# Performance work log

Hardware: AMD Instinct MI355X
Metric: run time of the kernel (lower is better)

Reference implementation:

```python
import jax, jax.numpy as jnp
import numpy as np

D_MODEL, D_K, D_V, N_HEADS = 1024, 64, 64, 16


def setup_inputs() -> dict:
    key = jax.random.key(0)
    ks = jax.random.split(key, 8)
    B, S = 2, 2048
    s = 0.02
    return {
        "x": jax.random.normal(ks[0], (B, S, D_MODEL), dtype=jnp.float32),
        "Wq": jax.random.normal(ks[1], (D_MODEL, N_HEADS * D_K), dtype=jnp.float32) * s,
        "bq": jnp.zeros((N_HEADS * D_K,), dtype=jnp.float32),
        "Wk": jax.random.normal(ks[2], (D_MODEL, N_HEADS * D_K), dtype=jnp.float32) * s,
        "bk": jnp.zeros((N_HEADS * D_K,), dtype=jnp.float32),
        "Wv": jax.random.normal(ks[3], (D_MODEL, N_HEADS * D_V), dtype=jnp.float32) * s,
        "bv": jnp.zeros((N_HEADS * D_V,), dtype=jnp.float32),
        "Wo": jax.random.normal(ks[4], (N_HEADS * D_V, D_MODEL), dtype=jnp.float32) * s,
    }


def reference(x, Wq, bq, Wk, bk, Wv, bv, Wo):
    B, S, _ = x.shape
    split = lambda t, d: t.reshape(B, S, N_HEADS, d).transpose(0, 2, 1, 3)  # [B,H,S,d]
    Q = split(x @ Wq + bq, D_K)
    K = split(x @ Wk + bk, D_K)
    V = split(x @ Wv + bv, D_V)
    scores = jnp.einsum("bhqd,bhkd->bhqk", Q / jnp.sqrt(jnp.float32(D_K)), K)
    # causal mask: x + (1 - 1/tril) == 0 on allowed, -inf on disallowed
    causal = jnp.tril(jnp.ones((S, S), dtype=bool))
    scores = jnp.where(causal, scores, -jnp.inf)
    attn = jax.nn.softmax(scores, axis=-1)
    out = jnp.einsum("bhqk,bhkd->bhqd", attn, V)  # [B,H,S,d_v]
    out = out.transpose(0, 2, 1, 3).reshape(B, S, N_HEADS * D_V)
    return out @ Wo
```

## Files before the change

### kernel.cpp

```cpp
#include <hip/hip_runtime.h>
#include <hip/hip_bf16.h>
#include <hip/hip_fp16.h>
#include <cstdint>

#define DEVINL __device__ __forceinline__

typedef __attribute__((ext_vector_type(4))) float floatx4;
typedef __attribute__((ext_vector_type(8))) __bf16 bf16x8;
typedef __attribute__((ext_vector_type(4))) _Float16 half4;
typedef __attribute__((ext_vector_type(8))) _Float16 half8;
typedef __attribute__((ext_vector_type(4))) unsigned short u16x4;

DEVINL floatx4 mfma_16x16x32(bf16x8 a, bf16x8 b, floatx4 c) {
  return __builtin_amdgcn_mfma_f32_16x16x32_bf16(a, b, c, 0, 0, 0);
}
DEVINL floatx4 mfma_16x16x16_f16(half4 a, half4 b, floatx4 c) {
  return __builtin_amdgcn_mfma_f32_16x16x16f16(a, b, c, 0, 0, 0);
}

DEVINL void async_copy16(const void* g, void* l) {
  __builtin_amdgcn_global_load_lds(
      (__attribute__((address_space(1))) void*)(void*)g,
      (__attribute__((address_space(3))) void*)l, 16, 0, 0);
}

#define QSCALE 0.18033688011112042f

#define VS(d, s) \
  ((d) * 128 + (((((s) >> 3)) ^ ((d) & 7)) << 4) + ((s) & 7) * 2)

__global__ void prep(const float* __restrict__ x, const float* __restrict__ Wq,
                     const float* __restrict__ Wk, const float* __restrict__ Wv,
                     const float* __restrict__ Wo,
                     __hip_bfloat16* __restrict__ xb,
                     __hip_bfloat16* __restrict__ Wt,
                     __hip_bfloat16* __restrict__ Wot) {
  const int z = blockIdx.z;
  const int tx = threadIdx.x, ty = threadIdx.y;
  if (z == 4) {
    const int bi = blockIdx.y * 32 + blockIdx.x;
    const int tid = ty * 32 + tx;
    const int base = bi * 4096 + tid * 4;
#pragma unroll
    for (int j = 0; j < 4; ++j) {
      const int i = base + j * 1024;
      const float4 v = *(const float4*)&x[i];
      xb[i + 0] = __float2bfloat16(v.x);
      xb[i + 1] = __float2bfloat16(v.y);
      xb[i + 2] = __float2bfloat16(v.z);
      xb[i + 3] = __float2bfloat16(v.w);
    }
    return;
  }
  __shared__ float tile[32][33];
  const float* W = (z == 0) ? Wq : (z == 1) ? Wk : (z == 2) ? Wv : Wo;
  __hip_bfloat16* dst = (z < 3) ? (Wt + ((int64_t)z << 20)) : Wot;
  const int k0 = blockIdx.x * 32, n0 = blockIdx.y * 32;
#pragma unroll
  for (int i = 0; i < 32; i += 8)
    tile[ty + i][tx] = W[(int64_t)(k0 + ty + i) * 1024 + n0 + tx];
  __syncthreads();
#pragma unroll
  for (int i = 0; i < 32; i += 8)
    dst[(int64_t)(n0 + ty + i) * 1024 + k0 + tx] =
        __float2bfloat16(tile[tx][ty + i]);
}

template <int MODE, int TM, int TN>
__global__ __launch_bounds__(256, 2) void gemm_bt(
    const __hip_bfloat16* __restrict__ A, const __hip_bfloat16* __restrict__ Bt,
    int M, int N, int K, const float* __restrict__ bq,
    const float* __restrict__ bk, const float* __restrict__ bv,
    __hip_bfloat16* __restrict__ Qb, __hip_bfloat16* __restrict__ Kb,
    _Float16* __restrict__ Vt, float* __restrict__ outf) {
  constexpr int MI = TM / 32, NJ = TN / 32;
  __shared__ __align__(16) char As[TM * 128];
  __shared__ __align__(16) char Bs[TN * 128];
  const int tid = threadIdx.x;
  const int wave = tid >> 6, lane = tid & 63;
  const int quad = lane >> 4, l16 = lane & 15;
  const int bm = blockIdx.x * TM, bn = blockIdx.y * TN;
  const int wm = (wave >> 1) * (TM / 2), wn = (wave & 1) * (TN / 2);
  const int sw = l16 & 7;

  floatx4 acc[MI][NJ] = {};

  for (int k0 = 0; k0 < K; k0 += 64) {
#pragma unroll
    for (int i = 0; i < TM / 32; ++i) {
      const int p = tid + i * 256;
      const int r = p >> 3, cc = (p & 7) ^ (r & 7);
      async_copy16(A + (int64_t)(bm + r) * K + k0 + cc * 8, As + p * 16);
    }
#pragma unroll
    for (int i = 0; i < TN / 32; ++i) {
      const int p = tid + i * 256;
      const int r = p >> 3, cc = (p & 7) ^ (r & 7);
      async_copy16(Bt + (int64_t)(bn + r) * K + k0 + cc * 8, Bs + p * 16);
    }
    __syncthreads();
    bf16x8 af[MI][2], bfr[NJ][2];
#pragma unroll
    for (int i = 0; i < MI; ++i)
#pragma unroll
      for (int h = 0; h < 2; ++h)
        af[i][h] = *(const bf16x8*)(As + (wm + i * 16 + l16) * 128 +
                                    (((h * 4 + quad) ^ sw) << 4));
#pragma unroll
    for (int j = 0; j < NJ; ++j)
#pragma unroll
      for (int h = 0; h < 2; ++h)
        bfr[j][h] = *(const bf16x8*)(Bs + (wn + j * 16 + l16) * 128 +
                                     (((h * 4 + quad) ^ sw) << 4));
#pragma unroll
    for (int i = 0; i < MI; ++i)
#pragma unroll
      for (int j = 0; j < NJ; ++j)
#pragma unroll
        for (int h = 0; h < 2; ++h)
          acc[i][j] = mfma_16x16x32(af[i][h], bfr[j][h], acc[i][j]);
    __syncthreads();
  }

  if (MODE == 1) {
#pragma unroll
    for (int i = 0; i < MI; ++i)
#pragma unroll
      for (int j = 0; j < NJ; ++j) {
        const int n = bn + wn + j * 16 + l16;
#pragma unroll
        for (int r = 0; r < 4; ++r) {
          const int m = bm + wm + i * 16 + quad * 4 + r;
          outf[(int64_t)m * N + n] = acc[i][j][r];
        }
      }
  } else if (bn < 2048) {
#pragma unroll
    for (int i = 0; i < MI; ++i)
#pragma unroll
      for (int j = 0; j < NJ; ++j) {
        const int n = bn + wn + j * 16 + l16;
        const int which = n >> 10, nn = n & 1023;
        const int h = nn >> 6, d = nn & 63;
        const float* bias = (which == 0) ? bq : bk;
#pragma unroll
        for (int r = 0; r < 4; ++r) {
          const int m = bm + wm + i * 16 + quad * 4 + r;
          const int b = m >> 11, s = m & 2047;
          float v = acc[i][j][r] + bias[nn];
          if (which == 0) v *= QSCALE;
          ((which == 0) ? Qb : Kb)[((int64_t)(b * 16 + h) * 2048 + s) * 64 + d] =
              __float2bfloat16(v);
        }
      }
  } else {
    char* scr = (wave & 1) ? Bs : As;
    const int h = ((bn + wn) & 1023) >> 6;
    const int bb = (bm + wm) >> 11;
    const int sbase = (bm + wm) & 2047;
    _Float16* dstV = Vt + (int64_t)(bb * 16 + h) * 64 * 2048;
#pragma unroll
    for (int phase = 0; phase < 2; ++phase) {
      __syncthreads();
      if ((wave >> 1) == phase) {
#pragma unroll
        for (int i = 0; i < 4; ++i)
#pragma unroll
          for (int j = 0; j < 4; ++j) {
            const int d = j * 16 + l16;
#pragma unroll
            for (int r = 0; r < 4; ++r) {
              const int s = i * 16 + quad * 4 + r;
              *(_Float16*)(scr + VS(d, s)) =
                  (_Float16)(acc[i][j][r] + bv[((bn + wn) & 1023) + d]);
            }
          }
      }
      __syncthreads();
      if ((wave >> 1) == phase) {
#pragma unroll
        for (int it = 0; it < 8; ++it) {
          const int idx = lane + it * 64;
          const int d = idx >> 3, sc = idx & 7;
          const half8 vv =
              *(const half8*)(scr + d * 128 + ((sc ^ (d & 7)) << 4));
          *(half8*)(dstV + (int64_t)d * 2048 + sbase + sc * 8) = vv;
        }
      }
    }
  }
}

__global__ __launch_bounds__(128, 2) void attn_kernel(
    const __hip_bfloat16* __restrict__ Qb, const __hip_bfloat16* __restrict__ Kb,
    const _Float16* __restrict__ Vt, __hip_bfloat16* __restrict__ Ab) {
  __shared__ __align__(16) char smem[32768];
  const int tid = threadIdx.x;
  const int wave = tid >> 6, lane = tid & 63;
  const int quad = lane >> 4, l16 = lane & 15;
  const int c = 31 - (int)(blockIdx.x >> 5);
  const int bh = blockIdx.x & 31;
  const int qbase = c * 64 + wave * 32;
  const int ktmax = c;

  const __hip_bfloat16* Qh = Qb + (int64_t)bh * 2048 * 64;
  const __hip_bfloat16* Kh = Kb + (int64_t)bh * 2048 * 64;
  const _Float16* Vh = Vt + (int64_t)bh * 64 * 2048;

  bf16x8 qf[2][2];
#pragma unroll
  for (int rt = 0; rt < 2; ++rt)
#pragma unroll
    for (int h = 0; h < 2; ++h)
      qf[rt][h] = *(const bf16x8*)&Qh[(int64_t)(qbase + rt * 16 + l16) * 64 +
                                      h * 32 + quad * 8];

  floatx4 o[2][4] = {};
  float lsum[2] = {0.f, 0.f};

  auto stage = [&](int buf, int k0s) {
#pragma unroll
    for (int i = 0; i < 4; ++i) {
      const int p = tid + i * 128;
      const int r = p >> 3, cc = (p & 7) ^ (r & 7);
      async_copy16(Kh + (int64_t)(k0s + r) * 64 + cc * 8,
                   smem + buf * 8192 + p * 16);
      async_copy16(Vh + (int64_t)r * 2048 + k0s + cc * 8,
                   smem + 16384 + buf * 8192 + p * 16);
    }
  };

  stage(0, 0);
  for (int kt = 0; kt <= ktmax; ++kt) {
    const int k0 = kt * 64;
    const int cur = kt & 1;
    __syncthreads();
    if (kt < ktmax) stage(cur ^ 1, k0 + 64);

    const char* kb = smem + cur * 8192;
    const char* vb = smem + 16384 + cur * 8192;
    const int sw = l16 & 7;

    bf16x8 kfr[4][2];
#pragma unroll
    for (int kk = 0; kk < 4; ++kk)
#pragma unroll
      for (int h = 0; h < 2; ++h)
        kfr[kk][h] = *(const bf16x8*)(kb + (kk * 16 + l16) * 128 +
                                      (((h * 4 + quad) ^ sw) << 4));

    floatx4 st[2][4];
#pragma unroll
    for (int kk = 0; kk < 4; ++kk)
#pragma unroll
      for (int rt = 0; rt < 2; ++rt) {
        floatx4 z = {};
        z = mfma_16x16x32(kfr[kk][0], qf[rt][0], z);
        st[rt][kk] = mfma_16x16x32(kfr[kk][1], qf[rt][1], z);
      }

    half4 vfr[4][4];
#pragma unroll
    for (int dt = 0; dt < 4; ++dt)
#pragma unroll
      for (int kk = 0; kk < 4; ++kk)
        vfr[dt][kk] = *(const half4*)(vb + (dt * 16 + l16) * 128 +
                                      (((kk * 2 + (quad >> 1)) ^ sw) << 4) +
                                      (quad & 1) * 8);

    const bool masked = (kt == ktmax);
    half4 pf[2][4];
#pragma unroll
    for (int rt = 0; rt < 2; ++rt) {
      const int qrow = qbase + rt * 16 + l16;
#pragma unroll
      for (int kk = 0; kk < 4; ++kk) {
#pragma unroll
        for (int r = 0; r < 4; ++r) {
          const int key = k0 + kk * 16 + quad * 4 + r;
          float p = __builtin_amdgcn_exp2f(st[rt][kk][r]);
          if (masked && key > qrow) p = 0.f;
          lsum[rt] += p;
          pf[rt][kk][r] = (_Float16)p;
        }
      }
    }

#pragma unroll
    for (int dt = 0; dt < 4; ++dt)
#pragma unroll
      for (int kk = 0; kk < 4; ++kk)
#pragma unroll
        for (int rt = 0; rt < 2; ++rt)
          o[rt][dt] = mfma_16x16x16_f16(vfr[dt][kk], pf[rt][kk], o[rt][dt]);
  }

#pragma unroll
  for (int rt = 0; rt < 2; ++rt) {
    lsum[rt] += __shfl_xor(lsum[rt], 16, 64);
    lsum[rt] += __shfl_xor(lsum[rt], 32, 64);
  }

  const int b = bh >> 4, h = bh & 15;
#pragma unroll
  for (int rt = 0; rt < 2; ++rt) {
    const float invl = 1.0f / lsum[rt];
#pragma unroll
    for (int dt = 0; dt < 4; ++dt) {
      u16x4 pack;
#pragma unroll
      for (int r = 0; r < 4; ++r)
        pack[r] = __builtin_bit_cast(unsigned short,
                                     __float2bfloat16(o[rt][dt][r] * invl));
      *(u16x4*)&Ab[(int64_t)(b * 2048 + qbase + rt * 16 + l16) * 1024 +
                   h * 64 + dt * 16 + quad * 4] = pack;
    }
  }
}

extern "C" void kernel_launch(void* const* d_in, const int* in_sizes, int n_in,
                              void* d_out, int out_size, void* d_ws,
                              size_t ws_size, hipStream_t stream) {
  const float* x = (const float*)d_in[0];
  const float* Wq = (const float*)d_in[1];
  const float* bq = (const float*)d_in[2];
  const float* Wk = (const float*)d_in[3];
  const float* bk = (const float*)d_in[4];
  const float* Wv = (const float*)d_in[5];
  const float* bv = (const float*)d_in[6];
  const float* Wo = (const float*)d_in[7];
  float* out = (float*)d_out;

  char* ws = (char*)d_ws;
  __hip_bfloat16* xb = (__hip_bfloat16*)(ws);
  __hip_bfloat16* Wt = (__hip_bfloat16*)(ws + (8ll << 20));
  __hip_bfloat16* Wot = (__hip_bfloat16*)(ws + (14ll << 20));
  __hip_bfloat16* Qb = (__hip_bfloat16*)(ws + (16ll << 20));
  __hip_bfloat16* Kb = (__hip_bfloat16*)(ws + (24ll << 20));
  _Float16* Vt = (_Float16*)(ws + (32ll << 20));
  __hip_bfloat16* Ab = xb;

  prep<<<dim3(32, 32, 5), dim3(32, 8), 0, stream>>>(x, Wq, Wk, Wv, Wo, xb, Wt,
                                                    Wot);
  gemm_bt<0, 128, 128><<<dim3(32, 24), 256, 0, stream>>>(
      xb, Wt, 4096, 3072, 1024, bq, bk, bv, Qb, Kb, Vt, nullptr);
  attn_kernel<<<dim3(1024), 128, 0, stream>>>(Qb, Kb, Vt, Ab);
  gemm_bt<1, 128, 64><<<dim3(32, 16), 256, 0, stream>>>(
      Ab, Wot, 4096, 1024, 1024, nullptr, nullptr, nullptr, nullptr, nullptr,
      nullptr, out);
}
```

Baseline: 168.0 us.

## Split causal attention key range into two segments and add combine kernel

Each query chunk's key range is split into two halves handled by separate blocks. Each block now has four waves of 16 query rows instead of two waves of 32 rows, which doubles the grid and evens out causal work across blocks. Each segment writes unnormalized fp16 partial outputs and row sums, and a new combine kernel adds the two partials and normalizes into the bf16 buffer the output projection reads. The intent is better occupancy and load balance, at the cost of an extra launch, extra global traffic for the partials, and duplicated K/V staging per segment.

```diff
diff --git a/kernel.cpp b/kernel.cpp
--- a/kernel.cpp
+++ b/kernel.cpp
@@ -191,37 +191,41 @@
   }
 }
 
-__global__ __launch_bounds__(128, 2) void attn_kernel(
+__global__ __launch_bounds__(256, 3) void attn_kernel(
     const __hip_bfloat16* __restrict__ Qb, const __hip_bfloat16* __restrict__ Kb,
-    const _Float16* __restrict__ Vt, __hip_bfloat16* __restrict__ Ab) {
+    const _Float16* __restrict__ Vt, _Float16* __restrict__ Ap0,
+    _Float16* __restrict__ Of1, float* __restrict__ L0,
+    float* __restrict__ L1) {
   __shared__ __align__(16) char smem[32768];
   const int tid = threadIdx.x;
   const int wave = tid >> 6, lane = tid & 63;
   const int quad = lane >> 4, l16 = lane & 15;
-  const int c = 31 - (int)(blockIdx.x >> 5);
+  const int idx = (int)(blockIdx.x >> 5);
   const int bh = blockIdx.x & 31;
-  const int qbase = c * 64 + wave * 32;
-  const int ktmax = c;
+  const int c = 31 - (idx >> 1);
+  const int seg = idx & 1;
+  const int nt = c + 1;
+  const int n0 = (nt + 1) >> 1;
+  const int ktmin = seg ? n0 : 0;
+  const int ktend = seg ? nt : n0;
+  const int qbase = c * 64 + wave * 16;
 
   const __hip_bfloat16* Qh = Qb + (int64_t)bh * 2048 * 64;
   const __hip_bfloat16* Kh = Kb + (int64_t)bh * 2048 * 64;
   const _Float16* Vh = Vt + (int64_t)bh * 64 * 2048;
 
-  bf16x8 qf[2][2];
-#pragma unroll
-  for (int rt = 0; rt < 2; ++rt)
-#pragma unroll
-    for (int h = 0; h < 2; ++h)
-      qf[rt][h] = *(const bf16x8*)&Qh[(int64_t)(qbase + rt * 16 + l16) * 64 +
-                                      h * 32 + quad * 8];
-
-  floatx4 o[2][4] = {};
-  float lsum[2] = {0.f, 0.f};
+  bf16x8 qf[2];
+#pragma unroll
+  for (int h = 0; h < 2; ++h)
+    qf[h] = *(const bf16x8*)&Qh[(int64_t)(qbase + l16) * 64 + h * 32 + quad * 8];
+
+  floatx4 o[4] = {};
+  float lsum = 0.f;
 
   auto stage = [&](int buf, int k0s) {
 #pragma unroll
-    for (int i = 0; i < 4; ++i) {
-      const int p = tid + i * 128;
+    for (int i = 0; i < 2; ++i) {
+      const int p = tid + i * 256;
       const int r = p >> 3, cc = (p & 7) ^ (r & 7);
       async_copy16(Kh + (int64_t)(k0s + r) * 64 + cc * 8,
                    smem + buf * 8192 + p * 16);
@@ -230,91 +234,106 @@
     }
   };
 
-  stage(0, 0);
-  for (int kt = 0; kt <= ktmax; ++kt) {
-    const int k0 = kt * 64;
-    const int cur = kt & 1;
-    __syncthreads();
-    if (kt < ktmax) stage(cur ^ 1, k0 + 64);
-
-    const char* kb = smem + cur * 8192;
-    const char* vb = smem + 16384 + cur * 8192;
-    const int sw = l16 & 7;
-
-    bf16x8 kfr[4][2];
-#pragma unroll
-    for (int kk = 0; kk < 4; ++kk)
-#pragma unroll
-      for (int h = 0; h < 2; ++h)
-        kfr[kk][h] = *(const bf16x8*)(kb + (kk * 16 + l16) * 128 +
-                                      (((h * 4 + quad) ^ sw) << 4));
-
-    floatx4 st[2][4];
-#pragma unroll
-    for (int kk = 0; kk < 4; ++kk)
-#pragma unroll
-      for (int rt = 0; rt < 2; ++rt) {
+  if (ktend > ktmin) {
+    stage(0, ktmin * 64);
+    for (int kt = ktmin; kt < ktend; ++kt) {
+      const int k0 = kt * 64;
+      const int cur = (kt - ktmin) & 1;
+      __syncthreads();
+      if (kt + 1 < ktend) stage(cur ^ 1, k0 + 64);
+
+      const char* kb = smem + cur * 8192;
+      const char* vb = smem + 16384 + cur * 8192;
+      const int sw = l16 & 7;
+
+      bf16x8 kfr[4][2];
+#pragma unroll
+      for (int kk = 0; kk < 4; ++kk)
+#pragma unroll
+        for (int h = 0; h < 2; ++h)
+          kfr[kk][h] = *(const bf16x8*)(kb + (kk * 16 + l16) * 128 +
+                                        (((h * 4 + quad) ^ sw) << 4));
+
+      floatx4 st[4];
+#pragma unroll
+      for (int kk = 0; kk < 4; ++kk) {
         floatx4 z = {};
-        z = mfma_16x16x32(kfr[kk][0], qf[rt][0], z);
-        st[rt][kk] = mfma_16x16x32(kfr[kk][1], qf[rt][1], z);
-      }
-
-    half4 vfr[4][4];
-#pragma unroll
-    for (int dt = 0; dt < 4; ++dt)
-#pragma unroll
-      for (int kk = 0; kk < 4; ++kk)
-        vfr[dt][kk] = *(const half4*)(vb + (dt * 16 + l16) * 128 +
-                                      (((kk * 2 + (quad >> 1)) ^ sw) << 4) +
-                                      (quad & 1) * 8);
-
-    const bool masked = (kt == ktmax);
-    half4 pf[2][4];
-#pragma unroll
-    for (int rt = 0; rt < 2; ++rt) {
-      const int qrow = qbase + rt * 16 + l16;
+        z = mfma_16x16x32(kfr[kk][0], qf[0], z);
+        st[kk] = mfma_16x16x32(kfr[kk][1], qf[1], z);
+      }
+
+      half4 vfr[4][4];
+#pragma unroll
+      for (int dt = 0; dt < 4; ++dt)
+#pragma unroll
+        for (int kk = 0; kk < 4; ++kk)
+          vfr[dt][kk] = *(const half4*)(vb + (dt * 16 + l16) * 128 +
+                                        (((kk * 2 + (quad >> 1)) ^ sw) << 4) +
+                                        (quad & 1) * 8);
+
+      const bool masked = (kt == c);
+      half4 pf[4];
 #pragma unroll
       for (int kk = 0; kk < 4; ++kk) {
 #pragma unroll
         for (int r = 0; r < 4; ++r) {
           const int key = k0 + kk * 16 + quad * 4 + r;
-          float p = __builtin_amdgcn_exp2f(st[rt][kk][r]);
-          if (masked && key > qrow) p = 0.f;
-          lsum[rt] += p;
-          pf[rt][kk][r] = (_Float16)p;
+          float p = __builtin_amdgcn_exp2f(st[kk][r]);
+          if (masked && key > qbase + l16) p = 0.f;
+          lsum += p;
+          pf[kk][r] = (_Float16)p;
         }
       }
-    }
-
-#pragma unroll
-    for (int dt = 0; dt < 4; ++dt)
-#pragma unroll
-      for (int kk = 0; kk < 4; ++kk)
-#pragma unroll
-        for (int rt = 0; rt < 2; ++rt)
-          o[rt][dt] = mfma_16x16x16_f16(vfr[dt][kk], pf[rt][kk], o[rt][dt]);
-  }
-
-#pragma unroll
-  for (int rt = 0; rt < 2; ++rt) {
-    lsum[rt] += __shfl_xor(lsum[rt], 16, 64);
-    lsum[rt] += __shfl_xor(lsum[rt], 32, 64);
-  }
+
+#pragma unroll
+      for (int dt = 0; dt < 4; ++dt)
+#pragma unroll
+        for (int kk = 0; kk < 4; ++kk)
+          o[dt] = mfma_16x16x16_f16(vfr[dt][kk], pf[kk], o[dt]);
+    }
+  }
+
+  lsum += __shfl_xor(lsum, 16, 64);
+  lsum += __shfl_xor(lsum, 32, 64);
+  const int chunk = bh * 32 + c;
+  if (quad == 0)
+    (seg ? L1 : L0)[chunk * 64 + wave * 16 + l16] = lsum;
 
   const int b = bh >> 4, h = bh & 15;
 #pragma unroll
-  for (int rt = 0; rt < 2; ++rt) {
-    const float invl = 1.0f / lsum[rt];
-#pragma unroll
-    for (int dt = 0; dt < 4; ++dt) {
-      u16x4 pack;
-#pragma unroll
-      for (int r = 0; r < 4; ++r)
-        pack[r] = __builtin_bit_cast(unsigned short,
-                                     __float2bfloat16(o[rt][dt][r] * invl));
-      *(u16x4*)&Ab[(int64_t)(b * 2048 + qbase + rt * 16 + l16) * 1024 +
-                   h * 64 + dt * 16 + quad * 4] = pack;
-    }
+  for (int dt = 0; dt < 4; ++dt) {
+    half4 pk;
+#pragma unroll
+    for (int r = 0; r < 4; ++r) pk[r] = (_Float16)o[dt][r];
+    if (seg == 0)
+      *(half4*)&Ap0[(int64_t)(b * 2048 + qbase + l16) * 1024 + h * 64 +
+                    dt * 16 + quad * 4] = pk;
+    else
+      *(half4*)&Of1[((int64_t)chunk * 64 + wave * 16 + l16) * 64 + dt * 16 +
+                    quad * 4] = pk;
+  }
+}
+
+__global__ void attn_combine(const _Float16* __restrict__ Ap0,
+                             const _Float16* __restrict__ Of1,
+                             const float* __restrict__ L0,
+                             const float* __restrict__ L1,
+                             __hip_bfloat16* __restrict__ Ab) {
+  const int chunk = blockIdx.x;
+  const int bh = chunk >> 5, c = chunk & 31;
+  const int b = bh >> 4, h = bh & 15;
+  const int qbase = c * 64;
+  const int t = threadIdx.x;
+  const int d = t & 63;
+#pragma unroll
+  for (int it = 0; it < 16; ++it) {
+    const int row = it * 4 + (t >> 6);
+    const float l = L0[chunk * 64 + row] + L1[chunk * 64 + row];
+    const int64_t a =
+        (int64_t)(b * 2048 + qbase + row) * 1024 + h * 64 + d;
+    const float o0 = (float)Ap0[a];
+    const float o1 = (float)Of1[((int64_t)chunk * 64 + row) * 64 + d];
+    Ab[a] = __float2bfloat16((o0 + o1) / l);
   }
 }
 
@@ -338,13 +357,18 @@
   __hip_bfloat16* Qb = (__hip_bfloat16*)(ws + (16ll << 20));
   __hip_bfloat16* Kb = (__hip_bfloat16*)(ws + (24ll << 20));
   _Float16* Vt = (_Float16*)(ws + (32ll << 20));
+  _Float16* Of1 = (_Float16*)(ws + (40ll << 20));
+  float* L0 = (float*)(ws + (8ll << 20));
+  float* L1 = (float*)(ws + (8ll << 20) + (256 << 10));
+  _Float16* Ap0 = (_Float16*)ws;
   __hip_bfloat16* Ab = xb;
 
   prep<<<dim3(32, 32, 5), dim3(32, 8), 0, stream>>>(x, Wq, Wk, Wv, Wo, xb, Wt,
                                                     Wot);
   gemm_bt<0, 128, 128><<<dim3(32, 24), 256, 0, stream>>>(
       xb, Wt, 4096, 3072, 1024, bq, bk, bv, Qb, Kb, Vt, nullptr);
-  attn_kernel<<<dim3(1024), 128, 0, stream>>>(Qb, Kb, Vt, Ab);
+  attn_kernel<<<dim3(2048), 256, 0, stream>>>(Qb, Kb, Vt, Ap0, Of1, L0, L1);
+  attn_combine<<<dim3(1024), 256, 0, stream>>>(Ap0, Of1, L0, L1, Ab);
   gemm_bt<1, 128, 64><<<dim3(32, 16), 256, 0, stream>>>(
       Ab, Wot, 4096, 1024, 1024, nullptr, nullptr, nullptr, nullptr, nullptr,
       nullptr, out);
```

New measurement: 173.5 us. 3.3% more time.
